# Kernel tuning notes

Measured on AMD Instinct MI355X. Metric: run time of the kernel, lower is better.

The kernel has to match this reference:

```python
import jax, jax.numpy as jnp
import numpy as np

M1, M2, BS = 2000, 400, 8
AT = M1 + M2
E1, E2, E3 = 60000, 20000, 20000
H, F, NG, L, C = 64, 64, 50, 4, 4
CUTOFF = 10.0
LOG2 = 0.6931471805599453  # shift of ShiftedSoftplus


def _ssp(x):
    return jax.nn.softplus(x) - LOG2


def _smear(d):
    # GaussianSmearing(0, cutoff, NG)
    offset = jnp.linspace(0.0, CUTOFF, NG)
    coeff = -0.5 / (offset[1] - offset[0]) ** 2
    return jnp.exp(coeff * (d[:, None] - offset[None, :]) ** 2)  # [E, NG]


def _colored_mlp(attr, colors, w1, b1, w2, b2):
    # w1:[C,NG,F] b1:[C,F] w2:[C,F,F] b2:[C,F]; route each edge through its color's MLP
    out = jnp.zeros((attr.shape[0], w1.shape[-1]), attr.dtype)
    for c in range(C):  # fixed small color count
        h = _ssp(attr @ w1[c] + b1[c]) @ w2[c] + b2[c]
        out = out + jnp.where((colors == c)[:, None], h, jnp.zeros((), attr.dtype))
    return out


def _block(h, ei, ew, attr, col, p):
    # InteractionBlock: CFConv -> ssp -> linear
    mw1, mb1, mw2, mb2, cw1, cw2, cb2, bw, bb = p
    Ccut = 0.5 * (jnp.cos(ew * jnp.pi / CUTOFF) + 1.0)
    W = _colored_mlp(attr, col, mw1, mb1, mw2, mb2) * Ccut[:, None]  # [E,F]
    x = h @ cw1                                   # lin1 (no bias) [N,F]
    msg = x[ei[:, 0]] * W                         # gather x_j, modulate
    agg = jax.ops.segment_sum(msg, ei[:, 1], num_segments=h.shape[0])  # scatter-add
    x = agg @ cw2 + cb2                           # lin2
    return _ssp(x) @ bw + bb                      # act + block linear


def _batch_graph(ei, ew, col):
    # replicate per-structure edges across the batch with node offset b*AT
    offs = (jnp.arange(BS, dtype=ei.dtype) * AT)[:, None, None]
    ei_b = (ei[None] + offs).reshape(-1, 2)
    return ei_b, jnp.tile(ew, BS), jnp.tile(col, BS)


def _forward(sites, sites_p, e1, ew1, c1, e2, ew2, c2, e3, ew3, c3,
             emb_w, emb_p_w, mlp_w1, mlp_b1, mlp_w2, mlp_b2,
             conv_w1, conv_w2, conv_b2, blk_w, blk_b,
             out_w1, out_b1, out_w2, out_b2):
    h = jnp.concatenate([emb_w[sites], emb_p_w[sites_p]], axis=1).reshape(BS * AT, H)
    graphs = []
    for (ei, ew, col) in ((e1, ew1, c1), (e2, ew2, c2), (e3, ew3, c3)):
        ei_b, ew_b, col_b = _batch_graph(ei, ew, col)
        graphs.append((ei_b, ew_b, col_b, _smear(ew_b)))
    for l in range(L):
        delta = jnp.zeros_like(h)
        for g, (ei_b, ew_b, col_b, attr_b) in enumerate(graphs):
            p = (mlp_w1[l, g], mlp_b1[l, g], mlp_w2[l, g], mlp_b2[l, g],
                 conv_w1[l, g], conv_w2[l, g], conv_b2[l, g], blk_w[l, g], blk_b[l, g])
            delta = delta + _block(h, ei_b, ew_b, attr_b, col_b, p)
        h = h + delta
    hp = h.reshape(BS, AT, H)[:, M1:, :]   # mask selects pore nodes only
    o = hp @ out_w1 + out_b1               # NB: original has `h - self.act(h)` no-op, so no activation here
    o = o @ out_w2 + out_b2                # [BS, M2, 1]
    return o.sum(axis=1)                   # 'add' readout per batch -> [BS, 1]


def setup_inputs() -> dict:
    key = jax.random.key(0)
    ks = jax.random.split(key, 24)
    f = lambda i, shape, s=0.1: jax.random.normal(ks[i], shape, jnp.float32) * s
    sites = jax.random.randint(ks[0], (BS, M1), 0, 1, dtype=jnp.int32)
    sites_p = jax.random.randint(ks[1], (BS, M2), 0, 2, dtype=jnp.int32)
    e1 = jax.random.randint(ks[2], (E1, 2), 0, M1, dtype=jnp.int32)
    e2 = jnp.stack([jax.random.randint(ks[3], (E2,), 0, M1, dtype=jnp.int32),
                    jax.random.randint(ks[4], (E2,), M1, AT, dtype=jnp.int32)], 1)
    e3 = jnp.stack([jax.random.randint(ks[5], (E3,), M1, AT, dtype=jnp.int32),
                    jax.random.randint(ks[6], (E3,), 0, M1, dtype=jnp.int32)], 1)
    ew1 = jax.random.uniform(ks[7], (E1,), jnp.float32, 0.5, CUTOFF)
    ew2 = jax.random.uniform(ks[8], (E2,), jnp.float32, 0.5, CUTOFF)
    ew3 = jax.random.uniform(ks[9], (E3,), jnp.float32, 0.5, CUTOFF)
    c1 = jax.random.randint(ks[10], (E1,), 0, C, dtype=jnp.int32)
    c2 = jax.random.randint(ks[11], (E2,), 0, C, dtype=jnp.int32)
    c3 = jax.random.randint(ks[12], (E3,), 0, C, dtype=jnp.int32)
    return {
        'sites': sites, 'sites_p': sites_p,
        'edge_idx1': e1, 'edge_weight1': ew1, 'colors1': c1,
        'edge_idx2': e2, 'edge_weight2': ew2, 'colors2': c2,
        'edge_idx3': e3, 'edge_weight3': ew3, 'colors3': c3,
        'emb_w': f(13, (1, H), 1.0), 'emb_p_w': f(14, (2, H), 1.0),
        'mlp_w1': f(15, (L, 3, C, NG, F)), 'mlp_b1': jnp.zeros((L, 3, C, F), jnp.float32),
        'mlp_w2': f(16, (L, 3, C, F, F)), 'mlp_b2': jnp.zeros((L, 3, C, F), jnp.float32),
        'conv_w1': f(17, (L, 3, H, F)), 'conv_w2': f(18, (L, 3, F, H)),
        'conv_b2': jnp.zeros((L, 3, H), jnp.float32),
        'blk_w': f(19, (L, 3, H, H)), 'blk_b': jnp.zeros((L, 3, H), jnp.float32),
        'out_w1': f(20, (H, H // 2)), 'out_b1': jnp.zeros((H // 2,), jnp.float32),
        'out_w2': f(21, (H // 2, 1)), 'out_b2': jnp.zeros((1,), jnp.float32),
    }


def reference(sites, sites_p, edge_idx1, edge_weight1, colors1,
              edge_idx2, edge_weight2, colors2, edge_idx3, edge_weight3, colors3,
              emb_w, emb_p_w, mlp_w1, mlp_b1, mlp_w2, mlp_b2,
              conv_w1, conv_w2, conv_b2, blk_w, blk_b,
              out_w1, out_b1, out_w2, out_b2):
    return _forward(sites, sites_p, edge_idx1, edge_weight1, colors1,
                    edge_idx2, edge_weight2, colors2, edge_idx3, edge_weight3, colors3,
                    emb_w, emb_p_w, mlp_w1, mlp_b1, mlp_w2, mlp_b2,
                    conv_w1, conv_w2, conv_b2, blk_w, blk_b,
                    out_w1, out_b1, out_w2, out_b2)
```

## Files before the change

### kernel.cpp

```cpp
#include <hip/hip_runtime.h>
#include <math.h>

constexpr int M1 = 2000, M2 = 400, BS = 8;
constexpr int AT = M1 + M2;
constexpr int NN = BS * AT;
constexpr int E1 = 60000, E2 = 20000, E3 = 20000;
constexpr int ET = E1 + E2 + E3;
constexpr int H = 64, F = 64, NG = 50, L = 4, C = 4;
constexpr float CUTOFF = 10.0f;
constexpr float LOG2F_ = 0.6931471805599453f;

constexpr float SMEAR_STEP = 10.0f / 49.0f;
constexpr float SMEAR_COEFF = -12.005f;
constexpr float PI_OVER_CUT = 0.31415926535897932f;

constexpr int NBLK = (ET + 255) / 256;

constexpr int NT = 256;
constexpr float DSCALE = (float)(NT - 1) / CUTOFF;

constexpr int TILE_M = 32;

constexpr int SITE_T = M1 / 4;
constexpr int PORE_T = M2 / 4;
constexpr int NTILE  = SITE_T + PORE_T;

constexpr int LT0 = M1 / 4;
constexpr int LT1 = M1 / 4;
constexpr int LT2 = M2 / 4;
constexpr int LTOT = LT0 + LT1 + LT2;

constexpr int A_TAB  = 48 * NT / 4;
constexpr int A_INIT = NN * 64 / 256;
constexpr int A_CNT  = NBLK;
constexpr int A_CV   = 3;
constexpr int A_TOT  = A_TAB + A_INIT + A_CNT + A_CV;
constexpr int B_PACK = 48 * NT * 64 / 256;
constexpr int B_TOT  = B_PACK + 3 + 2;

constexpr size_t O_HA    = 0;
constexpr size_t O_HB    = O_HA  + (size_t)NN * 64 * 4;
constexpr size_t O_XG    = O_HB  + (size_t)NN * 64 * 4;
constexpr size_t O_DG    = O_XG  + (size_t)3 * AT * 512 * 2;
constexpr size_t O_TAB2  = O_DG  + (size_t)3 * NN * 64 * 4;
constexpr size_t O_EDATA = O_TAB2 + (size_t)48 * NT * 64 * 4;
constexpr size_t O_INT   = O_EDATA + (size_t)ET * 16;
constexpr int I_DEG  = 0;
constexpr int I_CUR  = 7200;
constexpr int I_ZEND = 14400;
constexpr int I_BASE = 14400;
constexpr int I_PERM = 21616;
constexpr int I_CV   = 26016;

__device__ inline float sspf(float x) {
    return fmaxf(x, 0.0f) + log1pf(expf(-fabsf(x))) - LOG2F_;
}
__device__ inline float sspf_fast(float x) {
    float t = __expf(-fabsf(x));
    return fmaxf(x, 0.0f) + __logf(1.0f + t) - LOG2F_;
}

__device__ inline unsigned int bf16rn(float x) {
    unsigned int u = __float_as_uint(x);
    u = (u + 0x7FFFu + ((u >> 16) & 1u)) >> 16;
    return u & 0xFFFFu;
}

__device__ inline int graph_off(int g) { return g == 0 ? 0 : (g == 1 ? E1 : E1 + E2); }

__device__ inline void edge_decode(int idx, int& g, int& e,
                                   const int* ei1, const int* ei2, const int* ei3,
                                   const int* c1, const int* c2, const int* c3,
                                   const int*& ei, const int*& cl) {
    if (idx < E1)            { g = 0; e = idx;           ei = ei1; cl = c1; }
    else if (idx < E1 + E2)  { g = 1; e = idx - E1;      ei = ei2; cl = c2; }
    else                     { g = 2; e = idx - E1 - E2; ei = ei3; cl = c3; }
}

__global__ __launch_bounds__(256) void k_setupA(
    const float* __restrict__ mlp_w1, const float* __restrict__ mlp_b1,
    const float* __restrict__ mlp_w2, const float* __restrict__ mlp_b2,
    float* __restrict__ tabF,
    const int* __restrict__ sites, const int* __restrict__ sites_p,
    const float* __restrict__ emb_w, const float* __restrict__ emb_p_w,
    float* __restrict__ h,
    const int* __restrict__ ei1, const int* __restrict__ ei2,
    const int* __restrict__ ei3, const int* __restrict__ c1,
    const int* __restrict__ c2, const int* __restrict__ c3,
    int* __restrict__ deg,
    const float* __restrict__ conv_b2, const float* __restrict__ blk_w,
    const float* __restrict__ blk_b, float* __restrict__ cvbuf) {
    int bid = blockIdx.x;
    int t = threadIdx.x;
    if (bid < A_TAB) {
        const int lane = t & 63;
        int w = bid * 4 + (t >> 6);
        int s = w / NT;
        int p = w - s * NT;
        int l = s % L;
        int gc = s / L;
        int c = gc % C;
        int g = gc / C;
        float d = (float)p * (CUTOFF / (float)(NT - 1));
        size_t wb = (size_t)((l * 3 + g) * C + c);
        const float* w1 = mlp_w1 + wb * NG * F;
        const float* w2 = mlp_w2 + wb * F * F;
        float w1c[NG], w2c[F];
        #pragma unroll
        for (int k = 0; k < NG; k++) w1c[k] = w1[k * F + lane];
        #pragma unroll
        for (int k = 0; k < F; k++) w2c[k] = w2[k * F + lane];
        float b1c = mlp_b1[wb * F + lane];
        float b2c = mlp_b2[wb * F + lane];
        float dd = d - (float)lane * SMEAR_STEP;
        float av = (lane < NG) ? __expf(SMEAR_COEFF * dd * dd) : 0.0f;
        float acc = b1c;
        #pragma unroll
        for (int k = 0; k < NG; k++) acc = fmaf(__shfl(av, k), w1c[k], acc);
        float tt = sspf_fast(acc);
        float acc2 = b2c;
        #pragma unroll
        for (int j = 0; j < F; j++) acc2 = fmaf(__shfl(tt, j), w2c[j], acc2);
        float ccut = 0.5f * (__cosf(d * PI_OVER_CUT) + 1.0f);
        tabF[((size_t)s * NT + p) * 64 + lane] = acc2 * ccut;
    } else if (bid < A_TAB + A_INIT) {
        int idx = (bid - A_TAB) * 256 + t;
        int f = idx & 63;
        int n = idx >> 6;
        int b = n / AT;
        int i = n - b * AT;
        float v;
        if (i < M1) v = emb_w[sites[b * M1 + i] * H + f];
        else        v = emb_p_w[sites_p[b * M2 + (i - M1)] * H + f];
        h[idx] = v;
    } else if (bid < A_TAB + A_INIT + A_CNT) {
        int idx = (bid - A_TAB - A_INIT) * 256 + t;
        if (idx < ET) {
            int g, e; const int* ei; const int* cl;
            edge_decode(idx, g, e, ei1, ei2, ei3, c1, c2, c3, ei, cl);
            atomicAdd(&deg[g * AT + ei[2 * e + 1]], 1);
        }
    } else {
        int s = (bid - A_TAB - A_INIT - A_CNT) * 4 + (t >> 6);
        int lane = t & 63;
        if (s < 12) {
            float sl = sspf(conv_b2[s * 64 + lane]);
            const float* bw = blk_w + (size_t)s * 4096;
            float a = blk_b[s * 64 + lane];
            #pragma unroll 8
            for (int k = 0; k < 64; k++)
                a = fmaf(__shfl(sl, k), bw[k * 64 + lane], a);
            cvbuf[s * 64 + lane] = a;
        }
    }
}

__global__ __launch_bounds__(256) void k_setupB(
    const float* __restrict__ tabF, unsigned int* __restrict__ tab2,
    const int* __restrict__ deg, int* __restrict__ base,
    int* __restrict__ perm) {
    int bid = blockIdx.x;
    int t = threadIdx.x;
    if (bid < B_PACK) {
        int idx = bid * 256 + t;
        int pc = idx & (NT * 64 - 1);
        int nxt = (pc < (NT - 1) * 64) ? idx + 64 : idx;
        unsigned int lo = bf16rn(tabF[idx]);
        unsigned int hi = bf16rn(tabF[nxt]);
        tab2[idx] = lo | (hi << 16);
    } else if (bid < B_PACK + 3) {
        const int T = 256, CH = 10;
        __shared__ int lsum[256];
        int g = bid - B_PACK;
        int loc[CH];
        int s = 0;
        #pragma unroll
        for (int i = 0; i < CH; i++) {
            int idx = t * CH + i;
            int v = (idx < AT) ? deg[g * AT + idx] : 0;
            loc[i] = s;
            s += v;
        }
        lsum[t] = s;
        __syncthreads();
        for (int off = 1; off < T; off <<= 1) {
            int v = 0;
            if (t >= off) v = lsum[t - off];
            __syncthreads();
            lsum[t] += v;
            __syncthreads();
        }
        int tb = lsum[t] - s;
        #pragma unroll
        for (int i = 0; i < CH; i++) {
            int idx = t * CH + i;
            if (idx < AT) base[g * (AT + 1) + idx] = tb + loc[i];
        }
        if (t == T - 1) base[g * (AT + 1) + AT] = lsum[T - 1];
    } else {
        __shared__ int hist[256];
        __shared__ int cur[256];
        int q = bid - B_PACK - 3;
        int cnt   = q ? M2 : M1;
        int obase = q ? M1 : 0;
        hist[t] = 0;
        __syncthreads();
        for (int i = t; i < cnt; i += 256) {
            int key = q ? deg[AT + M1 + i] : (deg[i] + deg[2 * AT + i]);
            atomicAdd(&hist[min(key, 255)], 1);
        }
        __syncthreads();
        if (t == 0) {
            int run = 0;
            for (int k = 0; k < 256; k++) { cur[k] = run; run += hist[k]; }
        }
        __syncthreads();
        for (int i = t; i < cnt; i += 256) {
            int key = q ? deg[AT + M1 + i] : (deg[i] + deg[2 * AT + i]);
            int pos = atomicAdd(&cur[min(key, 255)], 1);
            perm[obase + pos] = q ? (M1 + i) : i;
        }
    }
}

__global__ void k_fill(const int* __restrict__ ei1, const int* __restrict__ ei2,
                       const int* __restrict__ ei3, const int* __restrict__ c1,
                       const int* __restrict__ c2, const int* __restrict__ c3,
                       const float* __restrict__ ew1, const float* __restrict__ ew2,
                       const float* __restrict__ ew3,
                       const int* __restrict__ base, int* __restrict__ cur,
                       int4* __restrict__ edata) {
    int idx = blockIdx.x * blockDim.x + threadIdx.x;
    if (idx >= ET) return;
    int g, e; const int* ei; const int* cl;
    edge_decode(idx, g, e, ei1, ei2, ei3, c1, c2, c3, ei, cl);
    const float* ew = (g == 0) ? ew1 : (g == 1 ? ew2 : ew3);
    int dst = ei[2 * e + 1];
    int src = ei[2 * e];
    int p = base[g * (AT + 1) + dst] + atomicAdd(&cur[g * AT + dst], 1);
    float t = ew[e] * DSCALE;
    int i0 = min((int)t, NT - 2);
    float fr = t - (float)i0;
    int cb = cl[e] * (L * NT) + i0;
    edata[graph_off(g) + p] = make_int4(src, cb, __float_as_int(fr), 0);
}

__device__ inline void fma4(float acc[4], float a, const float4 b) {
    acc[0] = fmaf(a, b.x, acc[0]);
    acc[1] = fmaf(a, b.y, acc[1]);
    acc[2] = fmaf(a, b.z, acc[2]);
    acc[3] = fmaf(a, b.w, acc[3]);
}

__device__ inline void stage_B(const float* __restrict__ gB, float (*Bs)[68], int t) {
    #pragma unroll
    for (int i = 0; i < 4; i++) {
        int v = t + i * 256;
        int r = v >> 4, c4 = (v & 15) * 4;
        *(float4*)&Bs[r][c4] = *(const float4*)(gB + (size_t)r * 64 + c4);
    }
}
__device__ inline void gemm_tile(const float (*As)[68], const float (*Bs)[68],
                                 int r0, int c0, float acc0[4], float acc1[4]) {
    #pragma unroll 4
    for (int k0 = 0; k0 < 64; k0 += 4) {
        float4 a0 = *(const float4*)&As[r0][k0];
        float4 a1 = *(const float4*)&As[r0 + 1][k0];
        float4 b0 = *(const float4*)&Bs[k0][c0];
        float4 b1 = *(const float4*)&Bs[k0 + 1][c0];
        float4 b2 = *(const float4*)&Bs[k0 + 2][c0];
        float4 b3 = *(const float4*)&Bs[k0 + 3][c0];
        fma4(acc0, a0.x, b0); fma4(acc0, a0.y, b1);
        fma4(acc0, a0.z, b2); fma4(acc0, a0.w, b3);
        fma4(acc1, a1.x, b0); fma4(acc1, a1.y, b1);
        fma4(acc1, a1.z, b2); fma4(acc1, a1.w, b3);
    }
}

__device__ inline void xg_transpose_store(const float (*T)[68],
                                          unsigned short* __restrict__ xg,
                                          int g, int i0, int t) {
    int k = t >> 6, c = t & 63;
    unsigned int w0 = bf16rn(T[k * 8 + 0][c]) | (bf16rn(T[k * 8 + 1][c]) << 16);
    unsigned int w1 = bf16rn(T[k * 8 + 2][c]) | (bf16rn(T[k * 8 + 3][c]) << 16);
    unsigned int w2 = bf16rn(T[k * 8 + 4][c]) | (bf16rn(T[k * 8 + 5][c]) << 16);
    unsigned int w3 = bf16rn(T[k * 8 + 6][c]) | (bf16rn(T[k * 8 + 7][c]) << 16);
    unsigned short* out = xg + (((size_t)g * AT + i0 + k) * 64 + c) * 8;
    *(uint4*)out = make_uint4(w0, w1, w2, w3);
}

__device__ inline void xg_tstore(const float (*T)[68],
                                 unsigned short* __restrict__ xg,
                                 int g, const int* __restrict__ perm,
                                 int pbase, int gi, int t) {
    int k = t >> 6, c = t & 63;
    int node = perm[pbase + gi * 4 + k];
    unsigned int w0 = bf16rn(T[k * 8 + 0][c]) | (bf16rn(T[k * 8 + 1][c]) << 16);
    unsigned int w1 = bf16rn(T[k * 8 + 2][c]) | (bf16rn(T[k * 8 + 3][c]) << 16);
    unsigned int w2 = bf16rn(T[k * 8 + 4][c]) | (bf16rn(T[k * 8 + 5][c]) << 16);
    unsigned int w3 = bf16rn(T[k * 8 + 6][c]) | (bf16rn(T[k * 8 + 7][c]) << 16);
    unsigned short* out = xg + (((size_t)g * AT + node) * 64 + c) * 8;
    *(uint4*)out = make_uint4(w0, w1, w2, w3);
}

__device__ inline void lin1_map(int bid, int& g, int& igrp) {
    if (bid < LT0)            { g = 0; igrp = bid; }
    else if (bid < LT0 + LT1) { g = 1; igrp = bid - LT0; }
    else                      { g = 2; igrp = LT0 + (bid - LT0 - LT1); }
}

__global__ __launch_bounds__(256) void k_lin1t(
    const float* __restrict__ h, const float* __restrict__ conv_w1,
    unsigned short* __restrict__ xg, int l) {
    __shared__ float As[TILE_M][68];
    __shared__ float Bs[64][68];
    int t = threadIdx.x;
    int g, igrp;
    lin1_map(blockIdx.x, g, igrp);
    int i0 = igrp * 4;
    #pragma unroll
    for (int it = 0; it < 2; it++) {
        int v = t + it * 256;
        int r = v >> 4, c4 = (v & 15) * 4;
        int n = (r & 7) * AT + i0 + (r >> 3);
        *(float4*)&As[r][c4] = *(const float4*)(h + (size_t)n * 64 + c4);
    }
    stage_B(conv_w1 + (size_t)(l * 3 + g) * 4096, Bs, t);
    __syncthreads();
    int cg = t & 15, rg = t >> 4;
    int c0 = cg * 4, r0 = rg * 2;
    float acc0[4] = {0, 0, 0, 0}, acc1[4] = {0, 0, 0, 0};
    gemm_tile(As, Bs, r0, c0, acc0, acc1);
    __syncthreads();
    *(float4*)&As[r0][c0]     = make_float4(acc0[0], acc0[1], acc0[2], acc0[3]);
    *(float4*)&As[r0 + 1][c0] = make_float4(acc1[0], acc1[1], acc1[2], acc1[3]);
    __syncthreads();
    xg_transpose_store(As, xg, g, i0, t);
}

__device__ inline void gather_dst(const int4* __restrict__ ed, int s, int e,
                                  const unsigned int* __restrict__ tg,
                                  const unsigned short* __restrict__ xgg,
                                  int lane, float acc[8]) {
    int i = s;
    while (i < e) {
        int cnt = min(e - i, 64);
        int4 mrec = ed[i + min(lane, cnt - 1)];
        int j = 0;
        for (; j + 2 <= cnt; j += 2) {
            int x0 = __shfl(mrec.x, j),     y0 = __shfl(mrec.y, j),     z0 = __shfl(mrec.z, j);
            int x1 = __shfl(mrec.x, j + 1), y1 = __shfl(mrec.y, j + 1), z1 = __shfl(mrec.z, j + 1);
            unsigned int u0 = tg[(size_t)y0 * 64 + lane];
            unsigned int u1 = tg[(size_t)y1 * 64 + lane];
            uint4 q0 = *(const uint4*)(xgg + ((size_t)x0 * 64 + lane) * 8);
            uint4 q1 = *(const uint4*)(xgg + ((size_t)x1 * 64 + lane) * 8);
            float lo0 = __uint_as_float(u0 << 16);
            float hi0 = __uint_as_float(u0 & 0xFFFF0000u);
            float lo1 = __uint_as_float(u1 << 16);
            float hi1 = __uint_as_float(u1 & 0xFFFF0000u);
            float wl0 = fmaf(__int_as_float(z0), hi0 - lo0, lo0);
            float wl1 = fmaf(__int_as_float(z1), hi1 - lo1, lo1);
            acc[0] = fmaf(__uint_as_float(q0.x << 16),         wl0, acc[0]);
            acc[1] = fmaf(__uint_as_float(q0.x & 0xFFFF0000u), wl0, acc[1]);
            acc[2] = fmaf(__uint_as_float(q0.y << 16),         wl0, acc[2]);
            acc[3] = fmaf(__uint_as_float(q0.y & 0xFFFF0000u), wl0, acc[3]);
            acc[4] = fmaf(__uint_as_float(q0.z << 16),         wl0, acc[4]);
            acc[5] = fmaf(__uint_as_float(q0.z & 0xFFFF0000u), wl0, acc[5]);
            acc[6] = fmaf(__uint_as_float(q0.w << 16),         wl0, acc[6]);
            acc[7] = fmaf(__uint_as_float(q0.w & 0xFFFF0000u), wl0, acc[7]);
            acc[0] = fmaf(__uint_as_float(q1.x << 16),         wl1, acc[0]);
            acc[1] = fmaf(__uint_as_float(q1.x & 0xFFFF0000u), wl1, acc[1]);
            acc[2] = fmaf(__uint_as_float(q1.y << 16),         wl1, acc[2]);
            acc[3] = fmaf(__uint_as_float(q1.y & 0xFFFF0000u), wl1, acc[3]);
            acc[4] = fmaf(__uint_as_float(q1.z << 16),         wl1, acc[4]);
            acc[5] = fmaf(__uint_as_float(q1.z & 0xFFFF0000u), wl1, acc[5]);
            acc[6] = fmaf(__uint_as_float(q1.w << 16),         wl1, acc[6]);
            acc[7] = fmaf(__uint_as_float(q1.w & 0xFFFF0000u), wl1, acc[7]);
        }
        if (j < cnt) {
            int x0 = __shfl(mrec.x, j), y0 = __shfl(mrec.y, j), z0 = __shfl(mrec.z, j);
            unsigned int u0 = tg[(size_t)y0 * 64 + lane];
            uint4 q = *(const uint4*)(xgg + ((size_t)x0 * 64 + lane) * 8);
            float lo0 = __uint_as_float(u0 << 16);
            float hi0 = __uint_as_float(u0 & 0xFFFF0000u);
            float wl = fmaf(__int_as_float(z0), hi0 - lo0, lo0);
            acc[0] = fmaf(__uint_as_float(q.x << 16),         wl, acc[0]);
            acc[1] = fmaf(__uint_as_float(q.x & 0xFFFF0000u), wl, acc[1]);
            acc[2] = fmaf(__uint_as_float(q.y << 16),         wl, acc[2]);
            acc[3] = fmaf(__uint_as_float(q.y & 0xFFFF0000u), wl, acc[3]);
            acc[4] = fmaf(__uint_as_float(q.z << 16),         wl, acc[4]);
            acc[5] = fmaf(__uint_as_float(q.z & 0xFFFF0000u), wl, acc[5]);
            acc[6] = fmaf(__uint_as_float(q.w << 16),         wl, acc[6]);
            acc[7] = fmaf(__uint_as_float(q.w & 0xFFFF0000u), wl, acc[7]);
        }
        i += cnt;
    }
}

__global__ __launch_bounds__(256) void k_layer(
    const int4* __restrict__ edata, const int* __restrict__ base,
    const int* __restrict__ perm,
    unsigned short* __restrict__ xg, const unsigned int* __restrict__ tab2,
    const float* __restrict__ conv_w2, const float* __restrict__ conv_b2,
    const float* __restrict__ blk_w, const float* __restrict__ blk_b,
    const float* __restrict__ conv_w1, const float* __restrict__ cvbuf,
    const float* __restrict__ hIn, float* __restrict__ hOut,
    int l, int last) {
    __shared__ float As[TILE_M][68];
    __shared__ float Bs[64][68];
    int t = threadIdx.x;
    const int lane = t & 63;
    const int wv = t >> 6;
    int bid = blockIdx.x;
    int site = (bid < SITE_T) ? 1 : 0;
    int gi = site ? (SITE_T - 1 - bid) : (PORE_T - 1 - (bid - SITE_T));
    int pbperm = site ? 0 : M1;
    int gA = site ? 0 : 1;
    int dst = perm[pbperm + gi * 4 + wv];
    size_t pbA = (size_t)(l * 3 + gA);
    stage_B(conv_w2 + pbA * 4096, Bs, t);

    float accA[8], accB[8];
    #pragma unroll
    for (int j = 0; j < 8; j++) { accA[j] = 0.0f; accB[j] = 0.0f; }
    {
        int s = base[gA * (AT + 1) + dst];
        int e = base[gA * (AT + 1) + dst + 1];
        gather_dst(edata + graph_off(gA), s, e,
                   tab2 + ((size_t)gA * C * L + l) * NT * 64,
                   xg + (size_t)gA * AT * 512, lane, accA);
    }
    if (site) {
        int s = base[2 * (AT + 1) + dst];
        int e = base[2 * (AT + 1) + dst + 1];
        gather_dst(edata + graph_off(2), s, e,
                   tab2 + ((size_t)2 * C * L + l) * NT * 64,
                   xg + (size_t)2 * AT * 512, lane, accB);
    }
    #pragma unroll
    for (int b = 0; b < 8; b++) As[wv * 8 + b][lane] = accA[b];
    __syncthreads();

    int cg = t & 15, rg = t >> 4;
    int c0 = cg * 4, r0 = rg * 2;
    float4 cbA = *(const float4*)(conv_b2 + pbA * 64 + c0);
    float x0[4] = {cbA.x, cbA.y, cbA.z, cbA.w};
    float x1[4] = {cbA.x, cbA.y, cbA.z, cbA.w};
    gemm_tile(As, Bs, r0, c0, x0, x1);
    __syncthreads();
    *(float4*)&As[r0][c0] =
        make_float4(sspf(x0[0]), sspf(x0[1]), sspf(x0[2]), sspf(x0[3]));
    *(float4*)&As[r0 + 1][c0] =
        make_float4(sspf(x1[0]), sspf(x1[1]), sspf(x1[2]), sspf(x1[3]));
    stage_B(blk_w + pbA * 4096, Bs, t);
    __syncthreads();

    int kk = r0 >> 3, b0 = r0 & 7;
    int nodek = perm[pbperm + gi * 4 + kk];
    size_t o0 = ((size_t)b0 * AT + nodek) * 64 + c0;
    size_t o1 = o0 + (size_t)AT * 64;
    float4 h0 = *(const float4*)(hIn + o0);
    float4 h1 = *(const float4*)(hIn + o1);
    const float* cvl = cvbuf + (size_t)l * 3 * 64;
    float4 bbA = *(const float4*)(blk_b + pbA * 64 + c0);
    float4 ex;
    if (site) {
        float4 bbB = *(const float4*)(blk_b + (size_t)(l * 3 + 2) * 64 + c0);
        float4 c1v = *(const float4*)(cvl + 64 + c0);
        ex = make_float4(bbB.x + c1v.x, bbB.y + c1v.y, bbB.z + c1v.z, bbB.w + c1v.w);
    } else {
        float4 c0v = *(const float4*)(cvl + c0);
        float4 c2v = *(const float4*)(cvl + 128 + c0);
        ex = make_float4(c0v.x + c2v.x, c0v.y + c2v.y, c0v.z + c2v.z, c0v.w + c2v.w);
    }
    float d0[4] = {h0.x + bbA.x + ex.x, h0.y + bbA.y + ex.y,
                   h0.z + bbA.z + ex.z, h0.w + bbA.w + ex.w};
    float d1[4] = {h1.x + bbA.x + ex.x, h1.y + bbA.y + ex.y,
                   h1.z + bbA.z + ex.z, h1.w + bbA.w + ex.w};
    gemm_tile(As, Bs, r0, c0, d0, d1);

    if (site) {
        __syncthreads();
        #pragma unroll
        for (int b = 0; b < 8; b++) As[wv * 8 + b][lane] = accB[b];
        stage_B(conv_w2 + (size_t)(l * 3 + 2) * 4096, Bs, t);
        __syncthreads();
        float4 cbB = *(const float4*)(conv_b2 + (size_t)(l * 3 + 2) * 64 + c0);
        float y0[4] = {cbB.x, cbB.y, cbB.z, cbB.w};
        float y1[4] = {cbB.x, cbB.y, cbB.z, cbB.w};
        gemm_tile(As, Bs, r0, c0, y0, y1);
        __syncthreads();
        *(float4*)&As[r0][c0] =
            make_float4(sspf(y0[0]), sspf(y0[1]), sspf(y0[2]), sspf(y0[3]));
        *(float4*)&As[r0 + 1][c0] =
            make_float4(sspf(y1[0]), sspf(y1[1]), sspf(y1[2]), sspf(y1[3]));
        stage_B(blk_w + (size_t)(l * 3 + 2) * 4096, Bs, t);
        __syncthreads();
        gemm_tile(As, Bs, r0, c0, d0, d1);
    }

    *(float4*)(hOut + o0) = make_float4(d0[0], d0[1], d0[2], d0[3]);
    *(float4*)(hOut + o1) = make_float4(d1[0], d1[1], d1[2], d1[3]);
    if (last) return;

    __syncthreads();
    *(float4*)&As[r0][c0]     = make_float4(d0[0], d0[1], d0[2], d0[3]);
    *(float4*)&As[r0 + 1][c0] = make_float4(d1[0], d1[1], d1[2], d1[3]);
    int gB = site ? 0 : 2;
    stage_B(conv_w1 + (size_t)((l + 1) * 3 + gB) * 4096, Bs, t);
    __syncthreads();
    float p0[4] = {0, 0, 0, 0}, p1[4] = {0, 0, 0, 0};
    gemm_tile(As, Bs, r0, c0, p0, p1);
    if (site) {
        __syncthreads();
        stage_B(conv_w1 + (size_t)((l + 1) * 3 + 1) * 4096, Bs, t);
        __syncthreads();
        float q0[4] = {0, 0, 0, 0}, q1[4] = {0, 0, 0, 0};
        gemm_tile(As, Bs, r0, c0, q0, q1);
        __syncthreads();
        *(float4*)&As[r0][c0]     = make_float4(p0[0], p0[1], p0[2], p0[3]);
        *(float4*)&As[r0 + 1][c0] = make_float4(p1[0], p1[1], p1[2], p1[3]);
        *(float4*)&Bs[r0][c0]     = make_float4(q0[0], q0[1], q0[2], q0[3]);
        *(float4*)&Bs[r0 + 1][c0] = make_float4(q1[0], q1[1], q1[2], q1[3]);
        __syncthreads();
        xg_tstore(As, xg, 0, perm, pbperm, gi, t);
        xg_tstore((const float(*)[68])Bs, xg, 1, perm, pbperm, gi, t);
    } else {
        __syncthreads();
        *(float4*)&As[r0][c0]     = make_float4(p0[0], p0[1], p0[2], p0[3]);
        *(float4*)&As[r0 + 1][c0] = make_float4(p1[0], p1[1], p1[2], p1[3]);
        __syncthreads();
        xg_tstore(As, xg, 2, perm, pbperm, gi, t);
    }
}

__global__ void k_read(const float* __restrict__ h,
                       const float* __restrict__ w1, const float* __restrict__ b1,
                       const float* __restrict__ w2, const float* __restrict__ b2,
                       float* __restrict__ out) {
    int b = blockIdx.x;
    int lane = threadIdx.x & 63;
    int wv = threadIdx.x >> 6;
    __shared__ float part[4];
    float weff = 0.0f;
    #pragma unroll
    for (int j = 0; j < H / 2; j++) weff = fmaf(w1[lane * (H / 2) + j], w2[j], weff);
    float acc = 0.0f;
    for (int i = wv * (M2 / 4); i < (wv + 1) * (M2 / 4); i++)
        acc += h[((size_t)b * AT + M1 + i) * H + lane];
    float v = acc * weff;
    for (int off = 32; off; off >>= 1) v += __shfl_xor(v, off);
    if (lane == 0) part[wv] = v;
    __syncthreads();
    if (threadIdx.x == 0) {
        float bias = b2[0];
        for (int j = 0; j < H / 2; j++) bias = fmaf(b1[j], w2[j], bias);
        out[b] = part[0] + part[1] + part[2] + part[3] + (float)M2 * bias;
    }
}

extern "C" void kernel_launch(void* const* d_in, const int* in_sizes, int n_in,
                              void* d_out, int out_size, void* d_ws, size_t ws_size,
                              hipStream_t stream) {
    const int* sites   = (const int*)d_in[0];
    const int* sites_p = (const int*)d_in[1];
    const int* ei1 = (const int*)d_in[2];
    const float* ew1 = (const float*)d_in[3];
    const int* c1 = (const int*)d_in[4];
    const int* ei2 = (const int*)d_in[5];
    const float* ew2 = (const float*)d_in[6];
    const int* c2 = (const int*)d_in[7];
    const int* ei3 = (const int*)d_in[8];
    const float* ew3 = (const float*)d_in[9];
    const int* c3 = (const int*)d_in[10];
    const float* emb_w   = (const float*)d_in[11];
    const float* emb_p_w = (const float*)d_in[12];
    const float* mlp_w1 = (const float*)d_in[13];
    const float* mlp_b1 = (const float*)d_in[14];
    const float* mlp_w2 = (const float*)d_in[15];
    const float* mlp_b2 = (const float*)d_in[16];
    const float* conv_w1 = (const float*)d_in[17];
    const float* conv_w2 = (const float*)d_in[18];
    const float* conv_b2 = (const float*)d_in[19];
    const float* blk_w = (const float*)d_in[20];
    const float* blk_b = (const float*)d_in[21];
    const float* out_w1 = (const float*)d_in[22];
    const float* out_b1 = (const float*)d_in[23];
    const float* out_w2 = (const float*)d_in[24];
    const float* out_b2 = (const float*)d_in[25];

    char* ws = (char*)d_ws;
    float* hA   = (float*)(ws + O_HA);
    float* hB   = (float*)(ws + O_HB);
    unsigned short* xg = (unsigned short*)(ws + O_XG);
    float* tabF = (float*)(ws + O_DG);
    unsigned int* tab2 = (unsigned int*)(ws + O_TAB2);
    int4*  edata = (int4*)(ws + O_EDATA);
    int* ip    = (int*)(ws + O_INT);
    int* deg   = ip + I_DEG;
    int* cur   = ip + I_CUR;
    int* ibase = ip + I_BASE;
    int* dperm = ip + I_PERM;
    float* cvbuf = (float*)(ip + I_CV);

    hipMemsetAsync(ip, 0, (size_t)I_ZEND * sizeof(int), stream);

    k_setupA<<<A_TOT, 256, 0, stream>>>(mlp_w1, mlp_b1, mlp_w2, mlp_b2, tabF,
                                        sites, sites_p, emb_w, emb_p_w, hA,
                                        ei1, ei2, ei3, c1, c2, c3, deg,
                                        conv_b2, blk_w, blk_b, cvbuf);
    k_setupB<<<B_TOT, 256, 0, stream>>>(tabF, tab2, deg, ibase, dperm);
    k_fill<<<NBLK, 256, 0, stream>>>(ei1, ei2, ei3, c1, c2, c3, ew1, ew2, ew3,
                                     ibase, cur, edata);

    k_lin1t<<<LTOT, 256, 0, stream>>>(hA, conv_w1, xg, 0);
    float* hcur = hA;
    float* hnxt = hB;
    for (int l = 0; l < L; l++) {
        int last = (l == L - 1) ? 1 : 0;
        k_layer<<<NTILE, 256, 0, stream>>>(edata, ibase, dperm, xg, tab2,
                                           conv_w2, conv_b2, blk_w, blk_b,
                                           conv_w1, cvbuf, hcur, hnxt, l, last);
        float* tmp = hcur; hcur = hnxt; hnxt = tmp;
    }
    k_read<<<BS, 256, 0, stream>>>(hcur, out_w1, out_b1, out_w2, out_b2, (float*)d_out);
}
```

Before: 323.1 us.

## Split layer gathers across two warp groups and merge fill with first lin1

The layer kernel now runs 512 threads. In site tiles the two graph gathers and their GEMM chains run concurrently on separate wave groups; in pore tiles the edge range is split between the two groups and the partial sums are added before lin2. The edge-fill kernel and the initial lin1 kernel are merged into one launch to remove a kernel boundary. The cost is double the shared memory per block, idle waves in pore tiles during the GEMMs, and possible occupancy limits.

```diff
diff --git a/kernel.cpp b/kernel.cpp
--- a/kernel.cpp
+++ b/kernel.cpp
@@ -64,6 +64,10 @@
     unsigned int u = __float_as_uint(x);
     u = (u + 0x7FFFu + ((u >> 16) & 1u)) >> 16;
     return u & 0xFFFFu;
+}
+
+__device__ inline float4 f4add(float4 a, float4 b) {
+    return make_float4(a.x + b.x, a.y + b.y, a.z + b.z, a.w + b.w);
 }
 
 __device__ inline int graph_off(int g) { return g == 0 ? 0 : (g == 1 ? E1 : E1 + E2); }
@@ -223,28 +227,6 @@
     }
 }
 
-__global__ void k_fill(const int* __restrict__ ei1, const int* __restrict__ ei2,
-                       const int* __restrict__ ei3, const int* __restrict__ c1,
-                       const int* __restrict__ c2, const int* __restrict__ c3,
-                       const float* __restrict__ ew1, const float* __restrict__ ew2,
-                       const float* __restrict__ ew3,
-                       const int* __restrict__ base, int* __restrict__ cur,
-                       int4* __restrict__ edata) {
-    int idx = blockIdx.x * blockDim.x + threadIdx.x;
-    if (idx >= ET) return;
-    int g, e; const int* ei; const int* cl;
-    edge_decode(idx, g, e, ei1, ei2, ei3, c1, c2, c3, ei, cl);
-    const float* ew = (g == 0) ? ew1 : (g == 1 ? ew2 : ew3);
-    int dst = ei[2 * e + 1];
-    int src = ei[2 * e];
-    int p = base[g * (AT + 1) + dst] + atomicAdd(&cur[g * AT + dst], 1);
-    float t = ew[e] * DSCALE;
-    int i0 = min((int)t, NT - 2);
-    float fr = t - (float)i0;
-    int cb = cl[e] * (L * NT) + i0;
-    edata[graph_off(g) + p] = make_int4(src, cb, __float_as_int(fr), 0);
-}
-
 __device__ inline void fma4(float acc[4], float a, const float4 b) {
     acc[0] = fmaf(a, b.x, acc[0]);
     acc[1] = fmaf(a, b.y, acc[1]);
@@ -276,6 +258,27 @@
         fma4(acc1, a1.z, b2); fma4(acc1, a1.w, b3);
     }
 }
+__device__ inline void gemm_tile_sum2(const float (*A0)[68], const float (*A1)[68],
+                                      const float (*Bs)[68],
+                                      int r0, int c0, float acc0[4], float acc1[4]) {
+    #pragma unroll 4
+    for (int k0 = 0; k0 < 64; k0 += 4) {
+        float4 p0 = *(const float4*)&A0[r0][k0];
+        float4 p1 = *(const float4*)&A1[r0][k0];
+        float4 q0 = *(const float4*)&A0[r0 + 1][k0];
+        float4 q1 = *(const float4*)&A1[r0 + 1][k0];
+        float4 a0 = f4add(p0, p1);
+        float4 a1 = f4add(q0, q1);
+        float4 b0 = *(const float4*)&Bs[k0][c0];
+        float4 b1 = *(const float4*)&Bs[k0 + 1][c0];
+        float4 b2 = *(const float4*)&Bs[k0 + 2][c0];
+        float4 b3 = *(const float4*)&Bs[k0 + 3][c0];
+        fma4(acc0, a0.x, b0); fma4(acc0, a0.y, b1);
+        fma4(acc0, a0.z, b2); fma4(acc0, a0.w, b3);
+        fma4(acc1, a1.x, b0); fma4(acc1, a1.y, b1);
+        fma4(acc1, a1.z, b2); fma4(acc1, a1.w, b3);
+    }
+}
 
 __device__ inline void xg_transpose_store(const float (*T)[68],
                                           unsigned short* __restrict__ xg,
@@ -301,41 +304,6 @@
     unsigned int w3 = bf16rn(T[k * 8 + 6][c]) | (bf16rn(T[k * 8 + 7][c]) << 16);
     unsigned short* out = xg + (((size_t)g * AT + node) * 64 + c) * 8;
     *(uint4*)out = make_uint4(w0, w1, w2, w3);
-}
-
-__device__ inline void lin1_map(int bid, int& g, int& igrp) {
-    if (bid < LT0)            { g = 0; igrp = bid; }
-    else if (bid < LT0 + LT1) { g = 1; igrp = bid - LT0; }
-    else                      { g = 2; igrp = LT0 + (bid - LT0 - LT1); }
-}
-
-__global__ __launch_bounds__(256) void k_lin1t(
-    const float* __restrict__ h, const float* __restrict__ conv_w1,
-    unsigned short* __restrict__ xg, int l) {
-    __shared__ float As[TILE_M][68];
-    __shared__ float Bs[64][68];
-    int t = threadIdx.x;
-    int g, igrp;
-    lin1_map(blockIdx.x, g, igrp);
-    int i0 = igrp * 4;
-    #pragma unroll
-    for (int it = 0; it < 2; it++) {
-        int v = t + it * 256;
-        int r = v >> 4, c4 = (v & 15) * 4;
-        int n = (r & 7) * AT + i0 + (r >> 3);
-        *(float4*)&As[r][c4] = *(const float4*)(h + (size_t)n * 64 + c4);
-    }
-    stage_B(conv_w1 + (size_t)(l * 3 + g) * 4096, Bs, t);
-    __syncthreads();
-    int cg = t & 15, rg = t >> 4;
-    int c0 = cg * 4, r0 = rg * 2;
-    float acc0[4] = {0, 0, 0, 0}, acc1[4] = {0, 0, 0, 0};
-    gemm_tile(As, Bs, r0, c0, acc0, acc1);
-    __syncthreads();
-    *(float4*)&As[r0][c0]     = make_float4(acc0[0], acc0[1], acc0[2], acc0[3]);
-    *(float4*)&As[r0 + 1][c0] = make_float4(acc1[0], acc1[1], acc1[2], acc1[3]);
-    __syncthreads();
-    xg_transpose_store(As, xg, g, i0, t);
 }
 
 __device__ inline void gather_dst(const int4* __restrict__ ed, int s, int e,
@@ -397,7 +365,7 @@
     }
 }
 
-__global__ __launch_bounds__(256) void k_layer(
+__global__ __launch_bounds__(512) void k_layer(
     const int4* __restrict__ edata, const int* __restrict__ base,
     const int* __restrict__ perm,
     unsigned short* __restrict__ xg, const unsigned int* __restrict__ tab2,
@@ -406,132 +374,207 @@
     const float* __restrict__ conv_w1, const float* __restrict__ cvbuf,
     const float* __restrict__ hIn, float* __restrict__ hOut,
     int l, int last) {
+    __shared__ float As[2][TILE_M][68];
+    __shared__ float Bs[2][64][68];
+    const int t = threadIdx.x;
+    const int lane = t & 63;
+    const int wv = t >> 6;
+    const int grp = wv >> 2;
+    const int t256 = t & 255;
+    const int bid = blockIdx.x;
+    const int site = (bid < SITE_T) ? 1 : 0;
+    const int gi = site ? (SITE_T - 1 - bid) : (PORE_T - 1 - (bid - SITE_T));
+    const int pbperm = site ? 0 : M1;
+    const size_t pb0 = (size_t)(l * 3 + (site ? 0 : 1));
+    const size_t pb1 = (size_t)(l * 3 + 2);
+
+    if (site || grp == 0)
+        stage_B(conv_w2 + (grp ? pb1 : pb0) * 4096, Bs[grp], t256);
+
+    {
+        float acc[8];
+        #pragma unroll
+        for (int j = 0; j < 8; j++) acc[j] = 0.0f;
+        int dstw = perm[pbperm + gi * 4 + (wv & 3)];
+        int gw = site ? (grp ? 2 : 0) : 1;
+        int s = base[gw * (AT + 1) + dstw];
+        int e = base[gw * (AT + 1) + dstw + 1];
+        if (!site) {
+            int mid = s + ((e - s + 1) >> 1);
+            if (grp == 0) e = mid; else s = mid;
+        }
+        gather_dst(edata + graph_off(gw), s, e,
+                   tab2 + ((size_t)gw * C * L + l) * NT * 64,
+                   xg + (size_t)gw * AT * 512, lane, acc);
+        int lw = wv & 3;
+        #pragma unroll
+        for (int b = 0; b < 8; b++) As[grp][lw * 8 + b][lane] = acc[b];
+    }
+    __syncthreads();
+
+    const int cg = t256 & 15, rg = t256 >> 4;
+    const int c0 = cg * 4, r0 = rg * 2;
+    const int kk = r0 >> 3, b0 = r0 & 7;
+    const int nodek = perm[pbperm + gi * 4 + kk];
+    const size_t o0 = ((size_t)b0 * AT + nodek) * 64 + c0;
+    const size_t o1 = o0 + (size_t)AT * 64;
+    const float* cvl = cvbuf + (size_t)l * 3 * 64;
+
+    float x0[4] = {0, 0, 0, 0}, x1[4] = {0, 0, 0, 0};
+    if (site || grp == 0) {
+        size_t pbg = grp ? pb1 : pb0;
+        float4 cb = *(const float4*)(conv_b2 + pbg * 64 + c0);
+        x0[0] = cb.x; x0[1] = cb.y; x0[2] = cb.z; x0[3] = cb.w;
+        x1[0] = cb.x; x1[1] = cb.y; x1[2] = cb.z; x1[3] = cb.w;
+        if (site) gemm_tile(As[grp], Bs[grp], r0, c0, x0, x1);
+        else      gemm_tile_sum2(As[0], As[1], Bs[0], r0, c0, x0, x1);
+    }
+    __syncthreads();
+    if (site || grp == 0) {
+        *(float4*)&As[grp][r0][c0] =
+            make_float4(sspf(x0[0]), sspf(x0[1]), sspf(x0[2]), sspf(x0[3]));
+        *(float4*)&As[grp][r0 + 1][c0] =
+            make_float4(sspf(x1[0]), sspf(x1[1]), sspf(x1[2]), sspf(x1[3]));
+        stage_B(blk_w + (grp ? pb1 : pb0) * 4096, Bs[grp], t256);
+    }
+    __syncthreads();
+
+    float d0[4] = {0, 0, 0, 0}, d1[4] = {0, 0, 0, 0};
+    if (grp == 0) {
+        float4 h0 = *(const float4*)(hIn + o0);
+        float4 h1 = *(const float4*)(hIn + o1);
+        float4 bb = *(const float4*)(blk_b + pb0 * 64 + c0);
+        float4 ex;
+        if (site) {
+            ex = *(const float4*)(cvl + 64 + c0);
+        } else {
+            float4 cv0 = *(const float4*)(cvl + c0);
+            float4 cv2 = *(const float4*)(cvl + 128 + c0);
+            ex = f4add(cv0, cv2);
+        }
+        d0[0] = h0.x + bb.x + ex.x; d0[1] = h0.y + bb.y + ex.y;
+        d0[2] = h0.z + bb.z + ex.z; d0[3] = h0.w + bb.w + ex.w;
+        d1[0] = h1.x + bb.x + ex.x; d1[1] = h1.y + bb.y + ex.y;
+        d1[2] = h1.z + bb.z + ex.z; d1[3] = h1.w + bb.w + ex.w;
+        gemm_tile(As[0], Bs[0], r0, c0, d0, d1);
+    } else if (site) {
+        float4 bb = *(const float4*)(blk_b + pb1 * 64 + c0);
+        d0[0] = bb.x; d0[1] = bb.y; d0[2] = bb.z; d0[3] = bb.w;
+        d1[0] = bb.x; d1[1] = bb.y; d1[2] = bb.z; d1[3] = bb.w;
+        gemm_tile(As[1], Bs[1], r0, c0, d0, d1);
+    }
+    __syncthreads();
+
+    if (site) {
+        if (grp == 1) {
+            *(float4*)&As[1][r0][c0]     = make_float4(d0[0], d0[1], d0[2], d0[3]);
+            *(float4*)&As[1][r0 + 1][c0] = make_float4(d1[0], d1[1], d1[2], d1[3]);
+            if (!last) stage_B(conv_w1 + (size_t)((l + 1) * 3 + 1) * 4096, Bs[1], t256);
+        } else if (!last) {
+            stage_B(conv_w1 + (size_t)((l + 1) * 3 + 0) * 4096, Bs[0], t256);
+        }
+        __syncthreads();
+        if (grp == 0) {
+            float4 e0 = *(const float4*)&As[1][r0][c0];
+            float4 e1 = *(const float4*)&As[1][r0 + 1][c0];
+            d0[0] += e0.x; d0[1] += e0.y; d0[2] += e0.z; d0[3] += e0.w;
+            d1[0] += e1.x; d1[1] += e1.y; d1[2] += e1.z; d1[3] += e1.w;
+            *(float4*)(hOut + o0) = make_float4(d0[0], d0[1], d0[2], d0[3]);
+            *(float4*)(hOut + o1) = make_float4(d1[0], d1[1], d1[2], d1[3]);
+            if (!last) {
+                *(float4*)&As[0][r0][c0]     = make_float4(d0[0], d0[1], d0[2], d0[3]);
+                *(float4*)&As[0][r0 + 1][c0] = make_float4(d1[0], d1[1], d1[2], d1[3]);
+            }
+        }
+        if (last) return;
+        __syncthreads();
+        float p0[4] = {0, 0, 0, 0}, p1[4] = {0, 0, 0, 0};
+        gemm_tile(As[0], Bs[grp], r0, c0, p0, p1);
+        __syncthreads();
+        *(float4*)&As[grp][r0][c0]     = make_float4(p0[0], p0[1], p0[2], p0[3]);
+        *(float4*)&As[grp][r0 + 1][c0] = make_float4(p1[0], p1[1], p1[2], p1[3]);
+        __syncthreads();
+        xg_tstore((const float(*)[68])As[grp], xg, grp ? 1 : 0, perm, pbperm, gi, t256);
+    } else {
+        if (grp == 0) {
+            *(float4*)(hOut + o0) = make_float4(d0[0], d0[1], d0[2], d0[3]);
+            *(float4*)(hOut + o1) = make_float4(d1[0], d1[1], d1[2], d1[3]);
+            if (!last) {
+                *(float4*)&As[0][r0][c0]     = make_float4(d0[0], d0[1], d0[2], d0[3]);
+                *(float4*)&As[0][r0 + 1][c0] = make_float4(d1[0], d1[1], d1[2], d1[3]);
+                stage_B(conv_w1 + (size_t)((l + 1) * 3 + 2) * 4096, Bs[0], t256);
+            }
+        }
+        if (last) return;
+        __syncthreads();
+        float p0[4] = {0, 0, 0, 0}, p1[4] = {0, 0, 0, 0};
+        if (grp == 0) gemm_tile(As[0], Bs[0], r0, c0, p0, p1);
+        __syncthreads();
+        if (grp == 0) {
+            *(float4*)&As[0][r0][c0]     = make_float4(p0[0], p0[1], p0[2], p0[3]);
+            *(float4*)&As[0][r0 + 1][c0] = make_float4(p1[0], p1[1], p1[2], p1[3]);
+        }
+        __syncthreads();
+        if (grp == 0)
+            xg_tstore((const float(*)[68])As[0], xg, 2, perm, pbperm, gi, t256);
+    }
+}
+
+__global__ __launch_bounds__(256) void k_fl(
+    const int* __restrict__ ei1, const int* __restrict__ ei2,
+    const int* __restrict__ ei3, const int* __restrict__ c1,
+    const int* __restrict__ c2, const int* __restrict__ c3,
+    const float* __restrict__ ew1, const float* __restrict__ ew2,
+    const float* __restrict__ ew3,
+    const int* __restrict__ base, int* __restrict__ cur,
+    int4* __restrict__ edata,
+    const float* __restrict__ h, const float* __restrict__ conv_w1,
+    unsigned short* __restrict__ xg) {
     __shared__ float As[TILE_M][68];
     __shared__ float Bs[64][68];
     int t = threadIdx.x;
-    const int lane = t & 63;
-    const int wv = t >> 6;
-    int bid = blockIdx.x;
-    int site = (bid < SITE_T) ? 1 : 0;
-    int gi = site ? (SITE_T - 1 - bid) : (PORE_T - 1 - (bid - SITE_T));
-    int pbperm = site ? 0 : M1;
-    int gA = site ? 0 : 1;
-    int dst = perm[pbperm + gi * 4 + wv];
-    size_t pbA = (size_t)(l * 3 + gA);
-    stage_B(conv_w2 + pbA * 4096, Bs, t);
-
-    float accA[8], accB[8];
+    if (blockIdx.x >= LTOT) {
+        int idx = (blockIdx.x - LTOT) * 256 + t;
+        if (idx >= ET) return;
+        int g, e; const int* ei; const int* cl;
+        edge_decode(idx, g, e, ei1, ei2, ei3, c1, c2, c3, ei, cl);
+        const float* ew = (g == 0) ? ew1 : (g == 1 ? ew2 : ew3);
+        int dst = ei[2 * e + 1];
+        int src = ei[2 * e];
+        int p = base[g * (AT + 1) + dst] + atomicAdd(&cur[g * AT + dst], 1);
+        float tt = ew[e] * DSCALE;
+        int i0 = min((int)tt, NT - 2);
+        float fr = tt - (float)i0;
+        int cb = cl[e] * (L * NT) + i0;
+        edata[graph_off(g) + p] = make_int4(src, cb, __float_as_int(fr), 0);
+        return;
+    }
+    int g, igrp;
+    {
+        int bid = blockIdx.x;
+        if (bid < LT0)            { g = 0; igrp = bid; }
+        else if (bid < LT0 + LT1) { g = 1; igrp = bid - LT0; }
+        else                      { g = 2; igrp = LT0 + (bid - LT0 - LT1); }
+    }
+    int i0 = igrp * 4;
     #pragma unroll
-    for (int j = 0; j < 8; j++) { accA[j] = 0.0f; accB[j] = 0.0f; }
-    {
-        int s = base[gA * (AT + 1) + dst];
-        int e = base[gA * (AT + 1) + dst + 1];
-        gather_dst(edata + graph_off(gA), s, e,
-                   tab2 + ((size_t)gA * C * L + l) * NT * 64,
-                   xg + (size_t)gA * AT * 512, lane, accA);
-    }
-    if (site) {
-        int s = base[2 * (AT + 1) + dst];
-        int e = base[2 * (AT + 1) + dst + 1];
-        gather_dst(edata + graph_off(2), s, e,
-                   tab2 + ((size_t)2 * C * L + l) * NT * 64,
-                   xg + (size_t)2 * AT * 512, lane, accB);
-    }
-    #pragma unroll
-    for (int b = 0; b < 8; b++) As[wv * 8 + b][lane] = accA[b];
-    __syncthreads();
-
+    for (int it = 0; it < 2; it++) {
+        int v = t + it * 256;
+        int r = v >> 4, c4 = (v & 15) * 4;
+        int n = (r & 7) * AT + i0 + (r >> 3);
+        *(float4*)&As[r][c4] = *(const float4*)(h + (size_t)n * 64 + c4);
+    }
+    stage_B(conv_w1 + (size_t)g * 4096, Bs, t);
+    __syncthreads();
     int cg = t & 15, rg = t >> 4;
     int c0 = cg * 4, r0 = rg * 2;
-    float4 cbA = *(const float4*)(conv_b2 + pbA * 64 + c0);
-    float x0[4] = {cbA.x, cbA.y, cbA.z, cbA.w};
-    float x1[4] = {cbA.x, cbA.y, cbA.z, cbA.w};
-    gemm_tile(As, Bs, r0, c0, x0, x1);
-    __syncthreads();
-    *(float4*)&As[r0][c0] =
-        make_float4(sspf(x0[0]), sspf(x0[1]), sspf(x0[2]), sspf(x0[3]));
-    *(float4*)&As[r0 + 1][c0] =
-        make_float4(sspf(x1[0]), sspf(x1[1]), sspf(x1[2]), sspf(x1[3]));
-    stage_B(blk_w + pbA * 4096, Bs, t);
-    __syncthreads();
-
-    int kk = r0 >> 3, b0 = r0 & 7;
-    int nodek = perm[pbperm + gi * 4 + kk];
-    size_t o0 = ((size_t)b0 * AT + nodek) * 64 + c0;
-    size_t o1 = o0 + (size_t)AT * 64;
-    float4 h0 = *(const float4*)(hIn + o0);
-    float4 h1 = *(const float4*)(hIn + o1);
-    const float* cvl = cvbuf + (size_t)l * 3 * 64;
-    float4 bbA = *(const float4*)(blk_b + pbA * 64 + c0);
-    float4 ex;
-    if (site) {
-        float4 bbB = *(const float4*)(blk_b + (size_t)(l * 3 + 2) * 64 + c0);
-        float4 c1v = *(const float4*)(cvl + 64 + c0);
-        ex = make_float4(bbB.x + c1v.x, bbB.y + c1v.y, bbB.z + c1v.z, bbB.w + c1v.w);
-    } else {
-        float4 c0v = *(const float4*)(cvl + c0);
-        float4 c2v = *(const float4*)(cvl + 128 + c0);
-        ex = make_float4(c0v.x + c2v.x, c0v.y + c2v.y, c0v.z + c2v.z, c0v.w + c2v.w);
-    }
-    float d0[4] = {h0.x + bbA.x + ex.x, h0.y + bbA.y + ex.y,
-                   h0.z + bbA.z + ex.z, h0.w + bbA.w + ex.w};
-    float d1[4] = {h1.x + bbA.x + ex.x, h1.y + bbA.y + ex.y,
-                   h1.z + bbA.z + ex.z, h1.w + bbA.w + ex.w};
-    gemm_tile(As, Bs, r0, c0, d0, d1);
-
-    if (site) {
-        __syncthreads();
-        #pragma unroll
-        for (int b = 0; b < 8; b++) As[wv * 8 + b][lane] = accB[b];
-        stage_B(conv_w2 + (size_t)(l * 3 + 2) * 4096, Bs, t);
-        __syncthreads();
-        float4 cbB = *(const float4*)(conv_b2 + (size_t)(l * 3 + 2) * 64 + c0);
-        float y0[4] = {cbB.x, cbB.y, cbB.z, cbB.w};
-        float y1[4] = {cbB.x, cbB.y, cbB.z, cbB.w};
-        gemm_tile(As, Bs, r0, c0, y0, y1);
-        __syncthreads();
-        *(float4*)&As[r0][c0] =
-            make_float4(sspf(y0[0]), sspf(y0[1]), sspf(y0[2]), sspf(y0[3]));
-        *(float4*)&As[r0 + 1][c0] =
-            make_float4(sspf(y1[0]), sspf(y1[1]), sspf(y1[2]), sspf(y1[3]));
-        stage_B(blk_w + (size_t)(l * 3 + 2) * 4096, Bs, t);
-        __syncthreads();
-        gemm_tile(As, Bs, r0, c0, d0, d1);
-    }
-
-    *(float4*)(hOut + o0) = make_float4(d0[0], d0[1], d0[2], d0[3]);
-    *(float4*)(hOut + o1) = make_float4(d1[0], d1[1], d1[2], d1[3]);
-    if (last) return;
-
-    __syncthreads();
-    *(float4*)&As[r0][c0]     = make_float4(d0[0], d0[1], d0[2], d0[3]);
-    *(float4*)&As[r0 + 1][c0] = make_float4(d1[0], d1[1], d1[2], d1[3]);
-    int gB = site ? 0 : 2;
-    stage_B(conv_w1 + (size_t)((l + 1) * 3 + gB) * 4096, Bs, t);
-    __syncthreads();
-    float p0[4] = {0, 0, 0, 0}, p1[4] = {0, 0, 0, 0};
-    gemm_tile(As, Bs, r0, c0, p0, p1);
-    if (site) {
-        __syncthreads();
-        stage_B(conv_w1 + (size_t)((l + 1) * 3 + 1) * 4096, Bs, t);
-        __syncthreads();
-        float q0[4] = {0, 0, 0, 0}, q1[4] = {0, 0, 0, 0};
-        gemm_tile(As, Bs, r0, c0, q0, q1);
-        __syncthreads();
-        *(float4*)&As[r0][c0]     = make_float4(p0[0], p0[1], p0[2], p0[3]);
-        *(float4*)&As[r0 + 1][c0] = make_float4(p1[0], p1[1], p1[2], p1[3]);
-        *(float4*)&Bs[r0][c0]     = make_float4(q0[0], q0[1], q0[2], q0[3]);
-        *(float4*)&Bs[r0 + 1][c0] = make_float4(q1[0], q1[1], q1[2], q1[3]);
-        __syncthreads();
-        xg_tstore(As, xg, 0, perm, pbperm, gi, t);
-        xg_tstore((const float(*)[68])Bs, xg, 1, perm, pbperm, gi, t);
-    } else {
-        __syncthreads();
-        *(float4*)&As[r0][c0]     = make_float4(p0[0], p0[1], p0[2], p0[3]);
-        *(float4*)&As[r0 + 1][c0] = make_float4(p1[0], p1[1], p1[2], p1[3]);
-        __syncthreads();
-        xg_tstore(As, xg, 2, perm, pbperm, gi, t);
-    }
+    float acc0[4] = {0, 0, 0, 0}, acc1[4] = {0, 0, 0, 0};
+    gemm_tile(As, Bs, r0, c0, acc0, acc1);
+    __syncthreads();
+    *(float4*)&As[r0][c0]     = make_float4(acc0[0], acc0[1], acc0[2], acc0[3]);
+    *(float4*)&As[r0 + 1][c0] = make_float4(acc1[0], acc1[1], acc1[2], acc1[3]);
+    __syncthreads();
+    xg_transpose_store(As, xg, g, i0, t);
 }
 
 __global__ void k_read(const float* __restrict__ h,
@@ -610,15 +653,15 @@
                                         ei1, ei2, ei3, c1, c2, c3, deg,
                                         conv_b2, blk_w, blk_b, cvbuf);
     k_setupB<<<B_TOT, 256, 0, stream>>>(tabF, tab2, deg, ibase, dperm);
-    k_fill<<<NBLK, 256, 0, stream>>>(ei1, ei2, ei3, c1, c2, c3, ew1, ew2, ew3,
-                                     ibase, cur, edata);
-
-    k_lin1t<<<LTOT, 256, 0, stream>>>(hA, conv_w1, xg, 0);
+    k_fl<<<LTOT + NBLK, 256, 0, stream>>>(ei1, ei2, ei3, c1, c2, c3,
+                                          ew1, ew2, ew3, ibase, cur, edata,
+                                          hA, conv_w1, xg);
+
     float* hcur = hA;
     float* hnxt = hB;
     for (int l = 0; l < L; l++) {
         int last = (l == L - 1) ? 1 : 0;
-        k_layer<<<NTILE, 256, 0, stream>>>(edata, ibase, dperm, xg, tab2,
+        k_layer<<<NTILE, 512, 0, stream>>>(edata, ibase, dperm, xg, tab2,
                                            conv_w2, conv_b2, blk_w, blk_b,
                                            conv_w1, cvbuf, hcur, hnxt, l, last);
         float* tmp = hcur; hcur = hnxt; hnxt = tmp;
```

After: 328.8 us. About the same (+1.8%).
